# Kernel tuning notes

Hardware: AMD Instinct MI355X
Metric: run time of the kernel (lower is better)

## Reference

```python
import jax, jax.numpy as jnp
import numpy as np

GRID = 128      # voxel grid extent per axis
NUM_BATCH = 4
N_PER = 25000   # points per scene (unique voxels)
C = 128
K = 32          # number of classes in probs
HEADS = 8
SCALE = 1.0


def setup_inputs() -> dict:
    key = jax.random.key(0)
    ks = jax.random.split(key, 12)
    N = NUM_BATCH * N_PER
    # unique voxel coordinates per scene (submanifold conv assumes no duplicate sites)
    coords_list = []
    for b in range(NUM_BATCH):
        flat = jax.random.permutation(jax.random.fold_in(ks[0], b), GRID ** 3)[:N_PER]
        xyz = jnp.stack([flat // (GRID * GRID), (flat // GRID) % GRID, flat % GRID], axis=1)
        bcol = jnp.full((N_PER, 1), b)
        coords_list.append(jnp.concatenate([bcol, xyz], axis=1))
    coords = jnp.concatenate(coords_list, axis=0).astype(jnp.int32)  # [N,4] = (b,x,y,z)
    feats = jax.random.normal(ks[1], (N, C), jnp.float32)
    probs = jax.random.normal(ks[2], (N, K), jnp.float32)
    conv_w = jax.random.normal(ks[3], (27, C, C), jnp.float32) * (1.0 / np.sqrt(27 * C))
    bn_gamma = 1.0 + 0.1 * jax.random.normal(ks[4], (C,), jnp.float32)
    bn_beta = 0.1 * jax.random.normal(ks[5], (C,), jnp.float32)
    in_proj_w = jax.random.normal(ks[6], (3 * C, C), jnp.float32) / np.sqrt(C)
    in_proj_b = 0.01 * jax.random.normal(ks[7], (3 * C,), jnp.float32)
    out_proj_w = jax.random.normal(ks[8], (C, C), jnp.float32) / np.sqrt(C)
    out_proj_b = 0.01 * jax.random.normal(ks[9], (C,), jnp.float32)
    bottleneck_w = jax.random.normal(ks[10], (C, 2 * C), jnp.float32) / np.sqrt(2 * C)
    return {"feats": feats, "probs": probs, "conv_w": conv_w, "bn_gamma": bn_gamma,
            "bn_beta": bn_beta, "in_proj_w": in_proj_w, "in_proj_b": in_proj_b,
            "out_proj_w": out_proj_w, "out_proj_b": out_proj_b,
            "bottleneck_w": bottleneck_w, "coords": coords, "batch_size": NUM_BATCH}


def _subm_conv3x3(feats, coords, conv_w, batch_size):
    """Submanifold 3x3x3 sparse conv: outputs only at active sites, gathering active neighbors."""
    N = feats.shape[0]
    b, xyz = coords[:, 0], coords[:, 1:]
    grid = jnp.full((batch_size, GRID, GRID, GRID), -1, jnp.int32)
    grid = grid.at[b, xyz[:, 0], xyz[:, 1], xyz[:, 2]].set(jnp.arange(N, dtype=jnp.int32))
    out = jnp.zeros((N, conv_w.shape[-1]), feats.dtype)
    kidx = 0
    for dx in (-1, 0, 1):
        for dy in (-1, 0, 1):
            for dz in (-1, 0, 1):
                nb = xyz + jnp.array([dx, dy, dz], jnp.int32)
                inb = jnp.all((nb >= 0) & (nb < GRID), axis=1)
                nbc = jnp.clip(nb, 0, GRID - 1)
                j = grid[b, nbc[:, 0], nbc[:, 1], nbc[:, 2]]
                ok = inb & (j >= 0)
                g = jnp.where(ok[:, None], feats[jnp.maximum(j, 0)], 0.0)
                out = out + g @ conv_w[kidx]
                kidx += 1
    return out


def _forward(feats, probs, conv_w, bn_gamma, bn_beta, in_proj_w, in_proj_b,
             out_proj_w, out_proj_b, bottleneck_w, coords, batch_size):
    N, Cc = feats.shape
    dh = Cc // HEADS
    b = coords[:, 0]
    # transform_input: SubMConv3d -> BatchNorm1d (batch stats) -> ReLU
    x = _subm_conv3x3(feats, coords, conv_w, batch_size)
    mu = jnp.mean(x, axis=0)
    var = jnp.var(x, axis=0)
    x = jax.nn.relu((x - mu) * jax.lax.rsqrt(var + 1e-5) * bn_gamma + bn_beta)
    # SpatialGatherModule: per-scene softmax over points, soft-weighted context [B,K,C]
    m = b[None, :] == jnp.arange(batch_size, dtype=b.dtype)[:, None]          # [B,N]
    neg = jnp.finfo(x.dtype).min
    z = jnp.where(m[:, :, None], (SCALE * probs)[None], neg)                  # [B,N,K]
    w = jax.nn.softmax(z, axis=1)
    ctx = jnp.einsum('bnk,nc->bkc', w, x)                                     # [B,K,C]
    # per-scene MultiheadAttention (unbatched): query = points, key/value = context
    Wq, Wk, Wv = in_proj_w[:Cc], in_proj_w[Cc:2 * Cc], in_proj_w[2 * Cc:]
    bq, bk, bv = in_proj_b[:Cc], in_proj_b[Cc:2 * Cc], in_proj_b[2 * Cc:]
    q = ((x @ Wq.T + bq) * (dh ** -0.5)).reshape(N, HEADS, dh)
    kh = (ctx @ Wk.T + bk).reshape(batch_size, -1, HEADS, dh)
    vh = (ctx @ Wv.T + bv).reshape(batch_size, -1, HEADS, dh)
    scores = jnp.einsum('nhd,bkhd->nbhk', q, kh)
    scores = scores[jnp.arange(N), b]                                         # [N,H,K] pick own scene
    attn = jax.nn.softmax(scores, axis=-1)
    o = jnp.einsum('nhk,bkhd->nbhd', attn, vh)[jnp.arange(N), b]              # [N,H,dh]
    attn_out = o.reshape(N, Cc) @ out_proj_w.T + out_proj_b
    # torch code aliases feats with inputs.features, so the in-place scatter makes
    # both halves of the concat equal to attn_out (literal forward semantics)
    y = jnp.concatenate([attn_out, attn_out], axis=1) @ bottleneck_w.T
    return y


def reference(feats, probs, conv_w, bn_gamma, bn_beta, in_proj_w, in_proj_b,
              out_proj_w, out_proj_b, bottleneck_w, coords, batch_size):
    return _forward(feats, probs, conv_w, bn_gamma, bn_beta, in_proj_w, in_proj_b,
                    out_proj_w, out_proj_b, bottleneck_w, coords, batch_size)
```

## Files before the change

kernel.cpp:

```cpp
#include <hip/hip_runtime.h>
#include <hip/hip_bf16.h>

typedef __attribute__((ext_vector_type(8))) short short8;
typedef __attribute__((ext_vector_type(4))) float floatx4;

#define NB 4
#define GRIDD 128
#define GRID3 (128*128*128)
#define C 128
#define KSLOT 32
#define CTX_BPB 256
#define DEN_BLK 1024
#define STAT_BLK 1024
#define PCAP 8192

static __device__ __forceinline__ unsigned short f2bf(float f){
  unsigned u = __builtin_bit_cast(unsigned, f);
  unsigned r = (u + 0x7FFFu + ((u >> 16) & 1u)) >> 16;
  return (unsigned short)r;
}
static __device__ __forceinline__ float bf2f(unsigned short h){
  unsigned u = ((unsigned)h) << 16;
  return __builtin_bit_cast(float, u);
}

__global__ void prepk(const float* __restrict__ feats, const float* __restrict__ convw,
                      const float* __restrict__ inw,
                      unsigned short* __restrict__ Fb, unsigned short* __restrict__ Wt,
                      unsigned short* __restrict__ Wq, unsigned short* __restrict__ WkvT,
                      long total1)
{
  const long stride = (long)gridDim.x * blockDim.x;
  const long i0 = (long)blockIdx.x * blockDim.x + threadIdx.x;
  const long q4 = total1 >> 2;
  const float4* f4 = reinterpret_cast<const float4*>(feats);
  ushort4* fb4 = reinterpret_cast<ushort4*>(Fb);
  for (long i = i0; i < q4; i += stride){
    const float4 v = f4[i];
    ushort4 o; o.x = f2bf(v.x); o.y = f2bf(v.y); o.z = f2bf(v.z); o.w = f2bf(v.w);
    fb4[i] = o;
  }
  for (long i = i0; i < 27L*C*C; i += stride){
    long k = i >> 14; long r = (i >> 7) & 127; long c = i & 127;
    Wt[i] = f2bf(convw[(k << 14) + (c << 7) + r]);
  }
  for (long i = i0; i < C*C; i += stride) Wq[i] = f2bf(inw[i]);
  for (long i = i0; i < 2L*C*C; i += stride){
    long which = i >> 14, rem = i & 16383, ii = rem >> 7, cout = rem & 127;
    WkvT[i] = f2bf(inw[((1 + which) << 14) + (cout << 7) + ii]);
  }
}

__global__ __launch_bounds__(128) void w2k(const float* __restrict__ bw,
                                           const float* __restrict__ outw,
                                           const float* __restrict__ outb,
                                           unsigned short* __restrict__ W2b,
                                           float* __restrict__ b2){
  const int o = blockIdx.x, i = threadIdx.x;
  __shared__ float wcf[128];
  __shared__ float red[128];
  const float w_i = bw[(size_t)o*256 + i] + bw[(size_t)o*256 + 128 + i];
  wcf[i] = w_i;
  red[i] = w_i * outb[i];
  __syncthreads();
  float acc = 0.f;
  #pragma unroll 8
  for (int j = 0; j < 128; j++) acc = fmaf(wcf[j], outw[j*128 + i], acc);
  W2b[o*128 + i] = f2bf(acc);
  for (int s = 64; s > 0; s >>= 1){
    if (i < s) red[i] += red[i + s];
    __syncthreads();
  }
  if (i == 0) b2[o] = red[0];
}

__global__ void scatterk(const int* __restrict__ coords, int* __restrict__ gh, int N){
  int p = blockIdx.x * 256 + threadIdx.x;
  if (p < N){
    int4 cr = *reinterpret_cast<const int4*>(coords + (size_t)p * 4);
    gh[(((cr.x*GRIDD + cr.y)*GRIDD + cr.z)*GRIDD) + cr.w] = p;
  }
}

__global__ __launch_bounds__(256) void pairk(const int* __restrict__ coords,
                                             const int* __restrict__ gh,
                                             int2* __restrict__ pairs,
                                             int* __restrict__ gcnt, int N){
  __shared__ int wcnt[4][27];
  __shared__ int woff[4][27];
  const int t = threadIdx.x, wave = t >> 6, lane = t & 63;
  const int p = blockIdx.x * 256 + t;
  const bool active = p < N;
  int4 cr = make_int4(0, 0, 0, 0);
  if (active) cr = *reinterpret_cast<const int4*>(coords + (size_t)p * 4);
  const int b = cr.x, x = cr.y, y = cr.z, z = cr.w;
  int jl[27];
  #pragma unroll
  for (int k = 0; k < 27; k++){
    jl[k] = -1;
    if (k == 13) continue;
    if (active){
      const int dx = k / 9 - 1, dy = (k / 3) % 3 - 1, dz = k % 3 - 1;
      const int nx = x + dx, ny = y + dy, nz = z + dz;
      if (((unsigned)nx < 128u) & ((unsigned)ny < 128u) & ((unsigned)nz < 128u)){
        const int gi = ((((b << 7) + nx) << 7) + ny) * GRIDD + nz;
        const int jj = gh[gi];
        if ((unsigned)jj < (unsigned)N){
          const int4 cj = *reinterpret_cast<const int4*>(coords + (size_t)jj * 4);
          if (cj.x == b && cj.y == nx && cj.z == ny && cj.w == nz) jl[k] = jj;
        }
      }
    }
  }
  #pragma unroll
  for (int k = 0; k < 27; k++){
    const unsigned long long m = __ballot(jl[k] >= 0);
    if (lane == 0) wcnt[wave][k] = (int)__popcll(m);
  }
  __syncthreads();
  if (t < 27){
    const int c0 = wcnt[0][t], c1 = wcnt[1][t], c2 = wcnt[2][t], c3 = wcnt[3][t];
    const int tot = c0 + c1 + c2 + c3;
    int gb = 0;
    if (t != 13 && tot > 0) gb = atomicAdd(&gcnt[t], tot);
    woff[0][t] = gb;
    woff[1][t] = gb + c0;
    woff[2][t] = gb + c0 + c1;
    woff[3][t] = gb + c0 + c1 + c2;
  }
  __syncthreads();
  const unsigned long long ltm = ((unsigned long long)1 << lane) - 1;
  #pragma unroll
  for (int k = 0; k < 27; k++){
    if (k == 13) continue;
    const unsigned long long m = __ballot(jl[k] >= 0);
    if (jl[k] >= 0){
      const int slot = woff[wave][k] + (int)__popcll(m & ltm);
      if (slot < PCAP) pairs[(size_t)k * PCAP + slot] = make_int2(p, jl[k]);
    }
  }
}

__global__ __launch_bounds__(256) void scatk(
    const unsigned short* __restrict__ F, const unsigned short* __restrict__ Wt,
    const int2* __restrict__ pairs, const int* __restrict__ gcnt,
    float* __restrict__ X, int N)
{
  __shared__ unsigned short wl[128 * 136];
  const int k = (blockIdx.x < 13) ? blockIdx.x : blockIdx.x + 1;
  const int t = threadIdx.x;
  const unsigned short* wg = Wt + (size_t)k * C * C;
  for (int idx = t; idx < 128 * 16; idx += 256){
    const int row = idx >> 4, seg = idx & 15;
    *reinterpret_cast<short8*>(&wl[row * 136 + seg * 8]) =
        *reinterpret_cast<const short8*>(wg + row * 128 + seg * 8);
  }
  __syncthreads();
  const int cnt = min(gcnt[k], PCAP);
  const int nch = (cnt + 15) >> 4;
  const int wave = t >> 6, lane = t & 63, lo = lane & 15, hi = lane >> 4;
  for (int c = blockIdx.y * 4 + wave; c < nch; c += 32 * 4){
    const int pidx = c * 16 + lo;
    const bool pv = pidx < cnt;
    const int2 pr = pv ? pairs[(size_t)k * PCAP + pidx] : make_int2(0, 0);
    const unsigned short* frow = F + (size_t)pr.y * C;
    short8 a[4];
    #pragma unroll
    for (int kc = 0; kc < 4; kc++){
      a[kc] = *reinterpret_cast<const short8*>(frow + kc * 32 + hi * 8);
      if (!pv) a[kc] = (short8){0,0,0,0,0,0,0,0};
    }
    floatx4 acc[8];
    #pragma unroll
    for (int i = 0; i < 8; i++) acc[i] = (floatx4){0.f,0.f,0.f,0.f};
    #pragma unroll
    for (int kc = 0; kc < 4; kc++){
      const int koff = kc * 32 + hi * 8;
      #pragma unroll
      for (int ct = 0; ct < 8; ct++){
        const short8 b = *reinterpret_cast<const short8*>(&wl[(ct*16 + lo) * 136 + koff]);
        acc[ct] = __builtin_amdgcn_mfma_f32_16x16x32_bf16(a[kc], b, acc[ct], 0, 0, 0);
      }
    }
    #pragma unroll
    for (int i2 = 0; i2 < 4; i2++){
      const int src = hi * 4 + i2;
      const int row = __shfl(pr.x, src);
      if (c * 16 + src < cnt){
        #pragma unroll
        for (int ct = 0; ct < 8; ct++)
          atomicAdd(&X[(size_t)row * C + ct * 16 + lo], acc[ct][i2]);
      }
    }
  }
}

__global__ __launch_bounds__(256) void denomk(const float* __restrict__ probs,
                                              const int* __restrict__ coords,
                                              float* __restrict__ dpart, int N){
  const int t = threadIdx.x, k = t & 31, rh = t >> 5;
  float a0 = 0.f, a1 = 0.f, a2 = 0.f, a3 = 0.f;
  for (int r = blockIdx.x * 8 + rh; r < N; r += DEN_BLK * 8){
    const int b = coords[(size_t)r * 4];
    const float e = __expf(probs[(size_t)r * 32 + k]);
    a0 += (b == 0) ? e : 0.f;
    a1 += (b == 1) ? e : 0.f;
    a2 += (b == 2) ? e : 0.f;
    a3 += (b == 3) ? e : 0.f;
  }
  __shared__ float ls[8][128];
  ls[rh][0*32 + k] = a0; ls[rh][1*32 + k] = a1;
  ls[rh][2*32 + k] = a2; ls[rh][3*32 + k] = a3;
  __syncthreads();
  if (t < 128){
    float s = 0.f;
    #pragma unroll
    for (int j = 0; j < 8; j++) s += ls[j][t];
    dpart[(size_t)blockIdx.x * 128 + t] = s;
  }
}

__global__ __launch_bounds__(256) void statsk(const float* __restrict__ X,
                                              float* __restrict__ spgs, int N){
  const int t = threadIdx.x, c4 = t & 31, rg = t >> 5;
  float s0=0.f,s1=0.f,s2=0.f,s3=0.f, q0=0.f,q1=0.f,q2=0.f,q3=0.f;
  for (int r = blockIdx.x * 8 + rg; r < N; r += STAT_BLK * 8){
    const float4 v = *reinterpret_cast<const float4*>(X + (size_t)r * C + c4 * 4);
    s0 += v.x; s1 += v.y; s2 += v.z; s3 += v.w;
    q0 = fmaf(v.x, v.x, q0); q1 = fmaf(v.y, v.y, q1);
    q2 = fmaf(v.z, v.z, q2); q3 = fmaf(v.w, v.w, q3);
  }
  __shared__ float ls[256][4], lq[256][4];
  ls[t][0]=s0; ls[t][1]=s1; ls[t][2]=s2; ls[t][3]=s3;
  lq[t][0]=q0; lq[t][1]=q1; lq[t][2]=q2; lq[t][3]=q3;
  __syncthreads();
  if (t < 32){
    float as[4]={0.f,0.f,0.f,0.f}, aq[4]={0.f,0.f,0.f,0.f};
    #pragma unroll
    for (int g = 0; g < 8; g++){
      #pragma unroll
      for (int j = 0; j < 4; j++){ as[j] += ls[g*32 + t][j]; aq[j] += lq[g*32 + t][j]; }
    }
    #pragma unroll
    for (int j = 0; j < 4; j++){
      spgs[(size_t)blockIdx.x * 256 + t*4 + j] = as[j];
      spgs[(size_t)blockIdx.x * 256 + 128 + t*4 + j] = aq[j];
    }
  }
}

__global__ __launch_bounds__(128) void reduk(const float* __restrict__ pgs,
                                             const float* __restrict__ dpart,
                                             float* __restrict__ gsum,
                                             float* __restrict__ gsq,
                                             float* __restrict__ denom){
  const int which = blockIdx.x, slice = blockIdx.y, t = threadIdx.x;
  float s = 0.f;
  if (which < 2){
    const float* src = pgs + which * 128 + t;
    for (int j = slice; j < STAT_BLK; j += 8) s += src[(size_t)j * 256];
    atomicAdd((which ? gsq : gsum) + t, s);
  } else {
    const float* src = dpart + t;
    for (int j = slice; j < DEN_BLK; j += 8) s += src[(size_t)j * 128];
    atomicAdd(denom + t, s);
  }
}

__global__ void finalizek(const float* __restrict__ sums, const float* __restrict__ sumsq,
                          const float* __restrict__ gamma, const float* __restrict__ beta,
                          const float* __restrict__ denom,
                          float* __restrict__ scalev, float* __restrict__ shiftv,
                          float* __restrict__ invden, int N){
  const int t = threadIdx.x;
  const float invN = 1.f / (float)N;
  const float mu = sums[t] * invN;
  const float var = sumsq[t] * invN - mu * mu;
  const float sc = gamma[t] * rsqrtf(var + 1e-5f);
  scalev[t] = sc;
  shiftv[t] = beta[t] - mu * sc;
  invden[t] = 1.f / denom[t];
}

__global__ __launch_bounds__(256) void ctx2k(const float* __restrict__ Xm,
                                             const float* __restrict__ probs,
                                             const float* __restrict__ scalev,
                                             const float* __restrict__ shiftv,
                                             float* __restrict__ pbuf, int NPER){
  __shared__ float xL[32 * 128];
  __shared__ float pe[32 * 32];
  __shared__ float red[2 * KSLOT * C];
  const int blk = blockIdx.x;
  const int b = blk >> 8, j = blk & 255;
  const int rows = (NPER + CTX_BPB - 1) / CTX_BPB;
  const int r0 = j * rows;
  const int r1 = min(r0 + rows, NPER);
  const int t = threadIdx.x, c = t & 127, rh = t >> 7;
  const float sc = scalev[c], sh = shiftv[c];
  float acc[KSLOT];
  #pragma unroll
  for (int k = 0; k < KSLOT; k++) acc[k] = 0.f;

  for (int base = r0; base < r1; base += 32){
    __syncthreads();
    #pragma unroll
    for (int i = 0; i < 4; i++){
      const int idx = i * 256 + t;
      const int r = idx >> 5, c4 = idx & 31;
      const int rr = base + r;
      float4 v = make_float4(0.f, 0.f, 0.f, 0.f);
      if (rr < r1) v = *reinterpret_cast<const float4*>(Xm + ((size_t)b * NPER + rr) * C + c4 * 4);
      *reinterpret_cast<float4*>(&xL[r * 128 + c4 * 4]) = v;
    }
    {
      const int r = t >> 3, k4 = t & 7;
      const int rr = base + r;
      float4 v = make_float4(0.f, 0.f, 0.f, 0.f);
      if (rr < r1){
        const float4 pv = *reinterpret_cast<const float4*>(probs + ((size_t)b * NPER + rr) * 32 + k4 * 4);
        v.x = __expf(pv.x); v.y = __expf(pv.y); v.z = __expf(pv.z); v.w = __expf(pv.w);
      }
      *reinterpret_cast<float4*>(&pe[r * 32 + k4 * 4]) = v;
    }
    __syncthreads();
    const int rend = min(32, r1 - base);
    for (int r = rh; r < rend; r += 2){
      const float xv = fmaxf(fmaf(xL[r * 128 + c], sc, sh), 0.f);
      const float4* wr = reinterpret_cast<const float4*>(&pe[r * 32]);
      #pragma unroll
      for (int kq = 0; kq < 8; kq++){
        const float4 w4 = wr[kq];
        acc[kq*4+0] = fmaf(w4.x, xv, acc[kq*4+0]);
        acc[kq*4+1] = fmaf(w4.y, xv, acc[kq*4+1]);
        acc[kq*4+2] = fmaf(w4.z, xv, acc[kq*4+2]);
        acc[kq*4+3] = fmaf(w4.w, xv, acc[kq*4+3]);
      }
    }
  }
  __syncthreads();
  #pragma unroll
  for (int k = 0; k < KSLOT; k++) red[(rh * KSLOT + k) * C + c] = acc[k];
  __syncthreads();
  float* dst = pbuf + (size_t)blk * KSLOT * C;
  for (int i = t; i < KSLOT * C; i += 256) dst[i] = red[i] + red[KSLOT * C + i];
}

__global__ __launch_bounds__(256) void kvk(const float* __restrict__ pbuf,
                                           const float* __restrict__ invden,
                                           const unsigned short* __restrict__ WkvT,
                                           const float* __restrict__ inb,
                                           float* __restrict__ kh, float* __restrict__ vh){
  __shared__ float rowp[2][C];
  __shared__ float row[C];
  const int bk = blockIdx.x;
  const int b = bk >> 5, k = bk & 31;
  const int t = threadIdx.x, c = t & 127, jh = t >> 7;
  float s = 0.f;
  for (int j = jh; j < CTX_BPB; j += 2)
    s += pbuf[((size_t)(b * CTX_BPB + j) * KSLOT + k) * C + c];
  rowp[jh][c] = s;
  __syncthreads();
  if (t < C) row[t] = (rowp[0][t] + rowp[1][t]) * invden[b * KSLOT + k];
  __syncthreads();
  const int which = t >> 7;
  const unsigned short* W = WkvT + (size_t)which * C * C;
  float acc = inb[(1 + which) * C + c];
  #pragma unroll 8
  for (int i = 0; i < C; i++) acc = fmaf(row[i], bf2f(W[i * C + c]), acc);
  (which ? vh : kh)[(size_t)bk * C + c] = acc;
}

__global__ __launch_bounds__(256) void gemm128(
    const unsigned short* __restrict__ A, const unsigned short* __restrict__ W,
    const float* __restrict__ bias, float scale,
    float* __restrict__ outF, unsigned short* __restrict__ outB, int N)
{
  const int tid = threadIdx.x;
  const int wave = tid >> 6, lane = tid & 63;
  const int rbase = blockIdx.x * 64 + (wave >> 1) * 32;
  const int cbase = (wave & 1) * 64;
  const int lo = lane & 15, hi = lane >> 4;
  floatx4 acc[2][4];
  #pragma unroll
  for (int rt = 0; rt < 2; rt++)
    #pragma unroll
    for (int ct = 0; ct < 4; ct++) acc[rt][ct] = (floatx4){0.f,0.f,0.f,0.f};
  const int m0 = rbase + lo, m1 = rbase + 16 + lo;
  const int m0c = m0 < N ? m0 : N - 1;
  const int m1c = m1 < N ? m1 : N - 1;
  #pragma unroll
  for (int kc = 0; kc < 4; kc++){
    const int koff = kc * 32 + hi * 8;
    const short8 a0 = *reinterpret_cast<const short8*>(A + (size_t)m0c * C + koff);
    const short8 a1 = *reinterpret_cast<const short8*>(A + (size_t)m1c * C + koff);
    #pragma unroll
    for (int ct = 0; ct < 4; ct++){
      const int n = cbase + ct * 16 + lo;
      const short8 b = *reinterpret_cast<const short8*>(W + (size_t)n * C + koff);
      acc[0][ct] = __builtin_amdgcn_mfma_f32_16x16x32_bf16(a0, b, acc[0][ct], 0, 0, 0);
      acc[1][ct] = __builtin_amdgcn_mfma_f32_16x16x32_bf16(a1, b, acc[1][ct], 0, 0, 0);
    }
  }
  #pragma unroll
  for (int rt = 0; rt < 2; rt++){
    #pragma unroll
    for (int ct = 0; ct < 4; ct++){
      const int col = cbase + ct * 16 + lo;
      const float bv = bias ? bias[col] : 0.f;
      #pragma unroll
      for (int i = 0; i < 4; i++){
        const int row = rbase + rt * 16 + hi * 4 + i;
        if (row < N){
          const float v = (acc[rt][ct][i] + bv) * scale;
          if (outF) outF[(size_t)row * C + col] = v;
          if (outB) outB[(size_t)row * C + col] = f2bf(v);
        }
      }
    }
  }
}

__global__ __launch_bounds__(256) void gemm128f(
    const float* __restrict__ A, const unsigned short* __restrict__ W,
    const float* __restrict__ bias, const float* __restrict__ bnsc,
    const float* __restrict__ bnsh, float scale,
    unsigned short* __restrict__ outB, int N)
{
  const int tid = threadIdx.x;
  const int wave = tid >> 6, lane = tid & 63;
  const int rbase = blockIdx.x * 64 + (wave >> 1) * 32;
  const int cbase = (wave & 1) * 64;
  const int lo = lane & 15, hi = lane >> 4;
  floatx4 acc[2][4];
  #pragma unroll
  for (int rt = 0; rt < 2; rt++)
    #pragma unroll
    for (int ct = 0; ct < 4; ct++) acc[rt][ct] = (floatx4){0.f,0.f,0.f,0.f};
  const int m0 = rbase + lo, m1 = rbase + 16 + lo;
  const int m0c = m0 < N ? m0 : N - 1;
  const int m1c = m1 < N ? m1 : N - 1;
  #pragma unroll
  for (int kc = 0; kc < 4; kc++){
    const int koff = kc * 32 + hi * 8;
    short8 a0, a1;
    #pragma unroll
    for (int half = 0; half < 2; half++){
      const float4 sc = *reinterpret_cast<const float4*>(bnsc + koff + half * 4);
      const float4 sh = *reinterpret_cast<const float4*>(bnsh + koff + half * 4);
      const float4 x0 = *reinterpret_cast<const float4*>(A + (size_t)m0c * C + koff + half * 4);
      const float4 x1 = *reinterpret_cast<const float4*>(A + (size_t)m1c * C + koff + half * 4);
      const float* scp = &sc.x; const float* shp = &sh.x;
      const float* x0p = &x0.x; const float* x1p = &x1.x;
      #pragma unroll
      for (int j = 0; j < 4; j++){
        a0[half*4 + j] = (short)f2bf(fmaxf(fmaf(x0p[j], scp[j], shp[j]), 0.f));
        a1[half*4 + j] = (short)f2bf(fmaxf(fmaf(x1p[j], scp[j], shp[j]), 0.f));
      }
    }
    #pragma unroll
    for (int ct = 0; ct < 4; ct++){
      const int n = cbase + ct * 16 + lo;
      const short8 b = *reinterpret_cast<const short8*>(W + (size_t)n * C + koff);
      acc[0][ct] = __builtin_amdgcn_mfma_f32_16x16x32_bf16(a0, b, acc[0][ct], 0, 0, 0);
      acc[1][ct] = __builtin_amdgcn_mfma_f32_16x16x32_bf16(a1, b, acc[1][ct], 0, 0, 0);
    }
  }
  #pragma unroll
  for (int rt = 0; rt < 2; rt++){
    #pragma unroll
    for (int ct = 0; ct < 4; ct++){
      const int col = cbase + ct * 16 + lo;
      const float bv = bias[col];
      #pragma unroll
      for (int i = 0; i < 4; i++){
        const int row = rbase + rt * 16 + hi * 4 + i;
        if (row < N) outB[(size_t)row * C + col] = f2bf((acc[rt][ct][i] + bv) * scale);
      }
    }
  }
}

__global__ __launch_bounds__(256) void attn3k(const unsigned short* __restrict__ qb,
                                              const float* __restrict__ kh,
                                              const float* __restrict__ vh,
                                              unsigned short* __restrict__ ob, int NPER){
  __shared__ float khL[KSLOT * C];
  __shared__ float vhL[KSLOT * C];
  const int t = threadIdx.x;
  const int b = blockIdx.y;
  const int n0 = blockIdx.x * 64;
  {
    const float4* ks = reinterpret_cast<const float4*>(kh + (size_t)b * KSLOT * C);
    const float4* vs = reinterpret_cast<const float4*>(vh + (size_t)b * KSLOT * C);
    float4* kd = reinterpret_cast<float4*>(khL);
    float4* vd = reinterpret_cast<float4*>(vhL);
    #pragma unroll
    for (int i = 0; i < 4; i++){ kd[i * 256 + t] = ks[i * 256 + t]; vd[i * 256 + t] = vs[i * 256 + t]; }
  }
  __syncthreads();
  const int h = t >> 5, p = t & 31;
  for (int g = 0; g < 2; g++){
    const int n = n0 + g * 32 + p;
    const int nc = n < NPER ? n : NPER - 1;
    float qv[16];
    {
      const short8* qp = reinterpret_cast<const short8*>(qb + ((size_t)b * NPER + nc) * C + h * 16);
      const short8 qa = qp[0], qc = qp[1];
      #pragma unroll
      for (int i = 0; i < 8; i++){
        qv[i]     = bf2f((unsigned short)qa[i]);
        qv[8 + i] = bf2f((unsigned short)qc[i]);
      }
    }
    float sv[KSLOT];
    #pragma unroll
    for (int k = 0; k < KSLOT; k++){
      const float4* kp = reinterpret_cast<const float4*>(&khL[k * C + h * 16]);
      const float4 k0 = kp[0], k1 = kp[1], k2 = kp[2], k3 = kp[3];
      float s;
      s = qv[0] * k0.x;
      s = fmaf(qv[1], k0.y, s);  s = fmaf(qv[2],  k0.z, s);  s = fmaf(qv[3],  k0.w, s);
      s = fmaf(qv[4], k1.x, s);  s = fmaf(qv[5],  k1.y, s);  s = fmaf(qv[6],  k1.z, s);
      s = fmaf(qv[7], k1.w, s);  s = fmaf(qv[8],  k2.x, s);  s = fmaf(qv[9],  k2.y, s);
      s = fmaf(qv[10], k2.z, s); s = fmaf(qv[11], k2.w, s);  s = fmaf(qv[12], k3.x, s);
      s = fmaf(qv[13], k3.y, s); s = fmaf(qv[14], k3.z, s);  s = fmaf(qv[15], k3.w, s);
      sv[k] = s;
    }
    float m = sv[0];
    #pragma unroll
    for (int k = 1; k < KSLOT; k++) m = fmaxf(m, sv[k]);
    float sum = 0.f;
    #pragma unroll
    for (int k = 0; k < KSLOT; k++){ const float e = __expf(sv[k] - m); sv[k] = e; sum += e; }
    const float inv = 1.f / sum;
    float o[16];
    #pragma unroll
    for (int i = 0; i < 16; i++) o[i] = 0.f;
    #pragma unroll
    for (int k = 0; k < KSLOT; k++){
      const float w = sv[k];
      const float4* vp = reinterpret_cast<const float4*>(&vhL[k * C + h * 16]);
      const float4 v0 = vp[0], v1 = vp[1], v2 = vp[2], v3 = vp[3];
      o[0]  = fmaf(w, v0.x, o[0]);  o[1]  = fmaf(w, v0.y, o[1]);
      o[2]  = fmaf(w, v0.z, o[2]);  o[3]  = fmaf(w, v0.w, o[3]);
      o[4]  = fmaf(w, v1.x, o[4]);  o[5]  = fmaf(w, v1.y, o[5]);
      o[6]  = fmaf(w, v1.z, o[6]);  o[7]  = fmaf(w, v1.w, o[7]);
      o[8]  = fmaf(w, v2.x, o[8]);  o[9]  = fmaf(w, v2.y, o[9]);
      o[10] = fmaf(w, v2.z, o[10]); o[11] = fmaf(w, v2.w, o[11]);
      o[12] = fmaf(w, v3.x, o[12]); o[13] = fmaf(w, v3.y, o[13]);
      o[14] = fmaf(w, v3.z, o[14]); o[15] = fmaf(w, v3.w, o[15]);
    }
    if (n < NPER){
      short8 s0, s1;
      #pragma unroll
      for (int i = 0; i < 8; i++){
        s0[i] = (short)f2bf(o[i] * inv);
        s1[i] = (short)f2bf(o[8 + i] * inv);
      }
      unsigned short* op = ob + ((size_t)b * NPER + n) * C + h * 16;
      *reinterpret_cast<short8*>(op) = s0;
      *reinterpret_cast<short8*>(op + 8) = s1;
    }
  }
}

extern "C" void kernel_launch(void* const* d_in, const int* in_sizes, int n_in,
                              void* d_out, int out_size, void* d_ws, size_t ws_size,
                              hipStream_t stream){
  const float* feats  = (const float*)d_in[0];
  const float* probs  = (const float*)d_in[1];
  const float* convw  = (const float*)d_in[2];
  const float* gamma  = (const float*)d_in[3];
  const float* beta   = (const float*)d_in[4];
  const float* inw    = (const float*)d_in[5];
  const float* inb    = (const float*)d_in[6];
  const float* outw   = (const float*)d_in[7];
  const float* outb   = (const float*)d_in[8];
  const float* bw     = (const float*)d_in[9];
  const int*   coords = (const int*)d_in[10];
  const int N = in_sizes[0] / C;
  const int NPER = N / NB;
  const int NBLK = (N + 63) / 64;

  char* ws = (char*)d_ws;
  size_t off = 0;
  auto alloc = [&](size_t bytes) -> char* {
    char* r = ws + off; off += (bytes + 255) & ~(size_t)255; return r;
  };
  int* grid_h            = (int*)alloc((size_t)NB * GRID3 * 4);
  unsigned short* featsb = (unsigned short*)alloc((size_t)N * C * 2);
  unsigned short* convwt = (unsigned short*)alloc((size_t)27 * C * C * 2);
  unsigned short* wq     = (unsigned short*)alloc((size_t)C * C * 2);
  unsigned short* wkvT   = (unsigned short*)alloc((size_t)2 * C * C * 2);
  unsigned short* w2b    = (unsigned short*)alloc((size_t)C * C * 2);
  float* b2              = (float*)alloc(512);
  float* xconv           = (float*)alloc((size_t)N * C * 4);
  unsigned short* qb     = (unsigned short*)alloc((size_t)N * C * 2);
  int2* pairs            = (int2*)alloc((size_t)27 * PCAP * 8);
  float* spgs            = (float*)alloc((size_t)STAT_BLK * 256 * 4);
  float* dpart           = (float*)alloc((size_t)DEN_BLK * 128 * 4);
  float* zero_base       = (float*)alloc((size_t)512 * 4);
  float* gsum   = zero_base;
  float* gsq    = zero_base + 128;
  float* denom  = zero_base + 256;
  int*   gcnt   = (int*)(zero_base + 384);
  float* invden = (float*)alloc(512);
  float* scalev = (float*)alloc(512);
  float* shiftv = (float*)alloc(512);
  float* kh     = (float*)alloc((size_t)NB * KSLOT * C * 4);
  float* vh     = (float*)alloc((size_t)NB * KSLOT * C * 4);
  float* pbuf = (float*)grid_h;
  unsigned short* o_bf = featsb;

  (void)hipMemsetAsync(zero_base, 0, (size_t)512 * 4, stream);
  prepk<<<2048, 256, 0, stream>>>(feats, convw, inw, featsb, convwt, wq, wkvT, (long)N * C);
  w2k<<<128, 128, 0, stream>>>(bw, outw, outb, w2b, b2);
  scatterk<<<(N + 255) / 256, 256, 0, stream>>>(coords, grid_h, N);
  pairk<<<(N + 255) / 256, 256, 0, stream>>>(coords, grid_h, pairs, gcnt, N);
  denomk<<<DEN_BLK, 256, 0, stream>>>(probs, coords, dpart, N);
  gemm128<<<NBLK, 256, 0, stream>>>(featsb, convwt + 13 * C * C, nullptr, 1.f, xconv, nullptr, N);
  scatk<<<dim3(26, 32), 256, 0, stream>>>(featsb, convwt, pairs, gcnt, xconv, N);
  statsk<<<STAT_BLK, 256, 0, stream>>>(xconv, spgs, N);
  {
    dim3 rg(3, 8);
    reduk<<<rg, 128, 0, stream>>>(spgs, dpart, gsum, gsq, denom);
  }
  finalizek<<<1, 128, 0, stream>>>(gsum, gsq, gamma, beta, denom, scalev, shiftv, invden, N);
  ctx2k<<<NB * CTX_BPB, 256, 0, stream>>>(xconv, probs, scalev, shiftv, pbuf, NPER);
  kvk<<<NB * KSLOT, 256, 0, stream>>>(pbuf, invden, wkvT, inb, kh, vh);
  gemm128f<<<NBLK, 256, 0, stream>>>(xconv, wq, inb, scalev, shiftv, 0.25f, qb, N);
  dim3 agrid((NPER + 63) / 64, NB);
  attn3k<<<agrid, 256, 0, stream>>>(qb, kh, vh, o_bf, NPER);
  gemm128<<<NBLK, 256, 0, stream>>>(o_bf, w2b, b2, 1.f, (float*)d_out, nullptr, N);
}
```

Measured before the change: 456.2 us.

## Emit bf16 copy of conv output in stats pass; interleave two queries in attention

The stats kernel now writes a bf16 copy of the conv output while it reads it. The context and Q-projection kernels then read this half-width copy instead of the fp32 tensor, which cuts the global traffic of those two later passes. The attention kernel also processes both query rows per thread at once, so each K/V value loaded from LDS is used twice and the dependent FMA chains run side by side. The cost is an extra write in statsk, bf16 rounding before batch-norm in ctx and Q, and higher register pressure in attention.

Result: slower. 1.183 ms (+159.3%).

```diff
diff --git a/kernel.cpp b/kernel.cpp
--- a/kernel.cpp
+++ b/kernel.cpp
@@ -221,11 +221,14 @@
 }
 
 __global__ __launch_bounds__(256) void statsk(const float* __restrict__ X,
-                                              float* __restrict__ spgs, int N){
+                                              float* __restrict__ spgs,
+                                              unsigned short* __restrict__ Xb, int N){
   const int t = threadIdx.x, c4 = t & 31, rg = t >> 5;
   float s0=0.f,s1=0.f,s2=0.f,s3=0.f, q0=0.f,q1=0.f,q2=0.f,q3=0.f;
   for (int r = blockIdx.x * 8 + rg; r < N; r += STAT_BLK * 8){
     const float4 v = *reinterpret_cast<const float4*>(X + (size_t)r * C + c4 * 4);
+    ushort4 o; o.x = f2bf(v.x); o.y = f2bf(v.y); o.z = f2bf(v.z); o.w = f2bf(v.w);
+    *reinterpret_cast<ushort4*>(Xb + (size_t)r * C + c4 * 4) = o;
     s0 += v.x; s1 += v.y; s2 += v.z; s3 += v.w;
     q0 = fmaf(v.x, v.x, q0); q1 = fmaf(v.y, v.y, q1);
     q2 = fmaf(v.z, v.z, q2); q3 = fmaf(v.w, v.w, q3);
@@ -282,7 +285,7 @@
   invden[t] = 1.f / denom[t];
 }
 
-__global__ __launch_bounds__(256) void ctx2k(const float* __restrict__ Xm,
+__global__ __launch_bounds__(256) void ctx2k(const unsigned short* __restrict__ Xb,
                                              const float* __restrict__ probs,
                                              const float* __restrict__ scalev,
                                              const float* __restrict__ shiftv,
@@ -304,13 +307,19 @@
   for (int base = r0; base < r1; base += 32){
     __syncthreads();
     #pragma unroll
-    for (int i = 0; i < 4; i++){
+    for (int i = 0; i < 2; i++){
       const int idx = i * 256 + t;
-      const int r = idx >> 5, c4 = idx & 31;
+      const int r = idx >> 4, c8 = idx & 15;
       const int rr = base + r;
-      float4 v = make_float4(0.f, 0.f, 0.f, 0.f);
-      if (rr < r1) v = *reinterpret_cast<const float4*>(Xm + ((size_t)b * NPER + rr) * C + c4 * 4);
-      *reinterpret_cast<float4*>(&xL[r * 128 + c4 * 4]) = v;
+      short8 v = (short8){0,0,0,0,0,0,0,0};
+      if (rr < r1) v = *reinterpret_cast<const short8*>(Xb + ((size_t)b * NPER + rr) * C + c8 * 8);
+      float4 f0, f1;
+      f0.x = bf2f((unsigned short)v[0]); f0.y = bf2f((unsigned short)v[1]);
+      f0.z = bf2f((unsigned short)v[2]); f0.w = bf2f((unsigned short)v[3]);
+      f1.x = bf2f((unsigned short)v[4]); f1.y = bf2f((unsigned short)v[5]);
+      f1.z = bf2f((unsigned short)v[6]); f1.w = bf2f((unsigned short)v[7]);
+      *reinterpret_cast<float4*>(&xL[r * 128 + c8 * 8]) = f0;
+      *reinterpret_cast<float4*>(&xL[r * 128 + c8 * 8 + 4]) = f1;
     }
     {
       const int r = t >> 3, k4 = t & 7;
@@ -420,8 +429,8 @@
   }
 }
 
-__global__ __launch_bounds__(256) void gemm128f(
-    const float* __restrict__ A, const unsigned short* __restrict__ W,
+__global__ __launch_bounds__(256) void gemm128b(
+    const unsigned short* __restrict__ A, const unsigned short* __restrict__ W,
     const float* __restrict__ bias, const float* __restrict__ bnsc,
     const float* __restrict__ bnsh, float scale,
     unsigned short* __restrict__ outB, int N)
@@ -442,20 +451,13 @@
   #pragma unroll
   for (int kc = 0; kc < 4; kc++){
     const int koff = kc * 32 + hi * 8;
-    short8 a0, a1;
-    #pragma unroll
-    for (int half = 0; half < 2; half++){
-      const float4 sc = *reinterpret_cast<const float4*>(bnsc + koff + half * 4);
-      const float4 sh = *reinterpret_cast<const float4*>(bnsh + koff + half * 4);
-      const float4 x0 = *reinterpret_cast<const float4*>(A + (size_t)m0c * C + koff + half * 4);
-      const float4 x1 = *reinterpret_cast<const float4*>(A + (size_t)m1c * C + koff + half * 4);
-      const float* scp = &sc.x; const float* shp = &sh.x;
-      const float* x0p = &x0.x; const float* x1p = &x1.x;
-      #pragma unroll
-      for (int j = 0; j < 4; j++){
-        a0[half*4 + j] = (short)f2bf(fmaxf(fmaf(x0p[j], scp[j], shp[j]), 0.f));
-        a1[half*4 + j] = (short)f2bf(fmaxf(fmaf(x1p[j], scp[j], shp[j]), 0.f));
-      }
+    short8 a0 = *reinterpret_cast<const short8*>(A + (size_t)m0c * C + koff);
+    short8 a1 = *reinterpret_cast<const short8*>(A + (size_t)m1c * C + koff);
+    #pragma unroll
+    for (int j = 0; j < 8; j++){
+      const float scj = bnsc[koff + j], shj = bnsh[koff + j];
+      a0[j] = (short)f2bf(fmaxf(fmaf(bf2f((unsigned short)a0[j]), scj, shj), 0.f));
+      a1[j] = (short)f2bf(fmaxf(fmaf(bf2f((unsigned short)a1[j]), scj, shj), 0.f));
     }
     #pragma unroll
     for (int ct = 0; ct < 4; ct++){
@@ -480,7 +482,7 @@
   }
 }
 
-__global__ __launch_bounds__(256) void attn3k(const unsigned short* __restrict__ qb,
+__global__ __launch_bounds__(256) void attn4k(const unsigned short* __restrict__ qb,
                                               const float* __restrict__ kh,
                                               const float* __restrict__ vh,
                                               unsigned short* __restrict__ ob, int NPER){
@@ -499,68 +501,103 @@
   }
   __syncthreads();
   const int h = t >> 5, p = t & 31;
-  for (int g = 0; g < 2; g++){
-    const int n = n0 + g * 32 + p;
-    const int nc = n < NPER ? n : NPER - 1;
-    float qv[16];
-    {
-      const short8* qp = reinterpret_cast<const short8*>(qb + ((size_t)b * NPER + nc) * C + h * 16);
-      const short8 qa = qp[0], qc = qp[1];
-      #pragma unroll
-      for (int i = 0; i < 8; i++){
-        qv[i]     = bf2f((unsigned short)qa[i]);
-        qv[8 + i] = bf2f((unsigned short)qc[i]);
-      }
-    }
-    float sv[KSLOT];
-    #pragma unroll
-    for (int k = 0; k < KSLOT; k++){
-      const float4* kp = reinterpret_cast<const float4*>(&khL[k * C + h * 16]);
-      const float4 k0 = kp[0], k1 = kp[1], k2 = kp[2], k3 = kp[3];
-      float s;
-      s = qv[0] * k0.x;
-      s = fmaf(qv[1], k0.y, s);  s = fmaf(qv[2],  k0.z, s);  s = fmaf(qv[3],  k0.w, s);
-      s = fmaf(qv[4], k1.x, s);  s = fmaf(qv[5],  k1.y, s);  s = fmaf(qv[6],  k1.z, s);
-      s = fmaf(qv[7], k1.w, s);  s = fmaf(qv[8],  k2.x, s);  s = fmaf(qv[9],  k2.y, s);
-      s = fmaf(qv[10], k2.z, s); s = fmaf(qv[11], k2.w, s);  s = fmaf(qv[12], k3.x, s);
-      s = fmaf(qv[13], k3.y, s); s = fmaf(qv[14], k3.z, s);  s = fmaf(qv[15], k3.w, s);
-      sv[k] = s;
-    }
-    float m = sv[0];
-    #pragma unroll
-    for (int k = 1; k < KSLOT; k++) m = fmaxf(m, sv[k]);
-    float sum = 0.f;
-    #pragma unroll
-    for (int k = 0; k < KSLOT; k++){ const float e = __expf(sv[k] - m); sv[k] = e; sum += e; }
-    const float inv = 1.f / sum;
-    float o[16];
-    #pragma unroll
-    for (int i = 0; i < 16; i++) o[i] = 0.f;
-    #pragma unroll
-    for (int k = 0; k < KSLOT; k++){
-      const float w = sv[k];
-      const float4* vp = reinterpret_cast<const float4*>(&vhL[k * C + h * 16]);
-      const float4 v0 = vp[0], v1 = vp[1], v2 = vp[2], v3 = vp[3];
-      o[0]  = fmaf(w, v0.x, o[0]);  o[1]  = fmaf(w, v0.y, o[1]);
-      o[2]  = fmaf(w, v0.z, o[2]);  o[3]  = fmaf(w, v0.w, o[3]);
-      o[4]  = fmaf(w, v1.x, o[4]);  o[5]  = fmaf(w, v1.y, o[5]);
-      o[6]  = fmaf(w, v1.z, o[6]);  o[7]  = fmaf(w, v1.w, o[7]);
-      o[8]  = fmaf(w, v2.x, o[8]);  o[9]  = fmaf(w, v2.y, o[9]);
-      o[10] = fmaf(w, v2.z, o[10]); o[11] = fmaf(w, v2.w, o[11]);
-      o[12] = fmaf(w, v3.x, o[12]); o[13] = fmaf(w, v3.y, o[13]);
-      o[14] = fmaf(w, v3.z, o[14]); o[15] = fmaf(w, v3.w, o[15]);
-    }
-    if (n < NPER){
-      short8 s0, s1;
-      #pragma unroll
-      for (int i = 0; i < 8; i++){
-        s0[i] = (short)f2bf(o[i] * inv);
-        s1[i] = (short)f2bf(o[8 + i] * inv);
-      }
-      unsigned short* op = ob + ((size_t)b * NPER + n) * C + h * 16;
-      *reinterpret_cast<short8*>(op) = s0;
-      *reinterpret_cast<short8*>(op + 8) = s1;
-    }
+  const int na = n0 + p, nb = n0 + 32 + p;
+  const int nac = na < NPER ? na : NPER - 1;
+  const int nbc = nb < NPER ? nb : NPER - 1;
+  float qa[16], qv[16];
+  {
+    const short8* qp = reinterpret_cast<const short8*>(qb + ((size_t)b * NPER + nac) * C + h * 16);
+    const short8 x0 = qp[0], x1 = qp[1];
+    const short8* qq = reinterpret_cast<const short8*>(qb + ((size_t)b * NPER + nbc) * C + h * 16);
+    const short8 y0 = qq[0], y1 = qq[1];
+    #pragma unroll
+    for (int i = 0; i < 8; i++){
+      qa[i] = bf2f((unsigned short)x0[i]); qa[8+i] = bf2f((unsigned short)x1[i]);
+      qv[i] = bf2f((unsigned short)y0[i]); qv[8+i] = bf2f((unsigned short)y1[i]);
+    }
+  }
+  float sa[KSLOT], sb[KSLOT];
+  #pragma unroll
+  for (int k = 0; k < KSLOT; k++){
+    const float4* kp = reinterpret_cast<const float4*>(&khL[k * C + h * 16]);
+    const float4 k0 = kp[0], k1 = kp[1], k2 = kp[2], k3 = kp[3];
+    const float* kf = &k0.x;
+    float s0 = 0.f, s1 = 0.f;
+    s0 = fmaf(qa[0], k0.x, s0); s1 = fmaf(qv[0], k0.x, s1);
+    s0 = fmaf(qa[1], k0.y, s0); s1 = fmaf(qv[1], k0.y, s1);
+    s0 = fmaf(qa[2], k0.z, s0); s1 = fmaf(qv[2], k0.z, s1);
+    s0 = fmaf(qa[3], k0.w, s0); s1 = fmaf(qv[3], k0.w, s1);
+    s0 = fmaf(qa[4], k1.x, s0); s1 = fmaf(qv[4], k1.x, s1);
+    s0 = fmaf(qa[5], k1.y, s0); s1 = fmaf(qv[5], k1.y, s1);
+    s0 = fmaf(qa[6], k1.z, s0); s1 = fmaf(qv[6], k1.z, s1);
+    s0 = fmaf(qa[7], k1.w, s0); s1 = fmaf(qv[7], k1.w, s1);
+    s0 = fmaf(qa[8], k2.x, s0); s1 = fmaf(qv[8], k2.x, s1);
+    s0 = fmaf(qa[9], k2.y, s0); s1 = fmaf(qv[9], k2.y, s1);
+    s0 = fmaf(qa[10], k2.z, s0); s1 = fmaf(qv[10], k2.z, s1);
+    s0 = fmaf(qa[11], k2.w, s0); s1 = fmaf(qv[11], k2.w, s1);
+    s0 = fmaf(qa[12], k3.x, s0); s1 = fmaf(qv[12], k3.x, s1);
+    s0 = fmaf(qa[13], k3.y, s0); s1 = fmaf(qv[13], k3.y, s1);
+    s0 = fmaf(qa[14], k3.z, s0); s1 = fmaf(qv[14], k3.z, s1);
+    s0 = fmaf(qa[15], k3.w, s0); s1 = fmaf(qv[15], k3.w, s1);
+    (void)kf;
+    sa[k] = s0; sb[k] = s1;
+  }
+  float ma = sa[0], mb = sb[0];
+  #pragma unroll
+  for (int k = 1; k < KSLOT; k++){ ma = fmaxf(ma, sa[k]); mb = fmaxf(mb, sb[k]); }
+  float suma = 0.f, sumb = 0.f;
+  #pragma unroll
+  for (int k = 0; k < KSLOT; k++){
+    const float ea = __expf(sa[k] - ma); sa[k] = ea; suma += ea;
+    const float eb = __expf(sb[k] - mb); sb[k] = eb; sumb += eb;
+  }
+  const float inva = 1.f / suma, invb = 1.f / sumb;
+  float oa[16], obv[16];
+  #pragma unroll
+  for (int i = 0; i < 16; i++){ oa[i] = 0.f; obv[i] = 0.f; }
+  #pragma unroll
+  for (int k = 0; k < KSLOT; k++){
+    const float wa = sa[k], wb = sb[k];
+    const float4* vp = reinterpret_cast<const float4*>(&vhL[k * C + h * 16]);
+    const float4 v0 = vp[0], v1 = vp[1], v2 = vp[2], v3 = vp[3];
+    oa[0]  = fmaf(wa, v0.x, oa[0]);  obv[0]  = fmaf(wb, v0.x, obv[0]);
+    oa[1]  = fmaf(wa, v0.y, oa[1]);  obv[1]  = fmaf(wb, v0.y, obv[1]);
+    oa[2]  = fmaf(wa, v0.z, oa[2]);  obv[2]  = fmaf(wb, v0.z, obv[2]);
+    oa[3]  = fmaf(wa, v0.w, oa[3]);  obv[3]  = fmaf(wb, v0.w, obv[3]);
+    oa[4]  = fmaf(wa, v1.x, oa[4]);  obv[4]  = fmaf(wb, v1.x, obv[4]);
+    oa[5]  = fmaf(wa, v1.y, oa[5]);  obv[5]  = fmaf(wb, v1.y, obv[5]);
+    oa[6]  = fmaf(wa, v1.z, oa[6]);  obv[6]  = fmaf(wb, v1.z, obv[6]);
+    oa[7]  = fmaf(wa, v1.w, oa[7]);  obv[7]  = fmaf(wb, v1.w, obv[7]);
+    oa[8]  = fmaf(wa, v2.x, oa[8]);  obv[8]  = fmaf(wb, v2.x, obv[8]);
+    oa[9]  = fmaf(wa, v2.y, oa[9]);  obv[9]  = fmaf(wb, v2.y, obv[9]);
+    oa[10] = fmaf(wa, v2.z, oa[10]); obv[10] = fmaf(wb, v2.z, obv[10]);
+    oa[11] = fmaf(wa, v2.w, oa[11]); obv[11] = fmaf(wb, v2.w, obv[11]);
+    oa[12] = fmaf(wa, v3.x, oa[12]); obv[12] = fmaf(wb, v3.x, obv[12]);
+    oa[13] = fmaf(wa, v3.y, oa[13]); obv[13] = fmaf(wb, v3.y, obv[13]);
+    oa[14] = fmaf(wa, v3.z, oa[14]); obv[14] = fmaf(wb, v3.z, obv[14]);
+    oa[15] = fmaf(wa, v3.w, oa[15]); obv[15] = fmaf(wb, v3.w, obv[15]);
+  }
+  if (na < NPER){
+    short8 s0, s1;
+    #pragma unroll
+    for (int i = 0; i < 8; i++){
+      s0[i] = (short)f2bf(oa[i] * inva);
+      s1[i] = (short)f2bf(oa[8 + i] * inva);
+    }
+    unsigned short* op = ob + ((size_t)b * NPER + na) * C + h * 16;
+    *reinterpret_cast<short8*>(op) = s0;
+    *reinterpret_cast<short8*>(op + 8) = s1;
+  }
+  if (nb < NPER){
+    short8 s0, s1;
+    #pragma unroll
+    for (int i = 0; i < 8; i++){
+      s0[i] = (short)f2bf(obv[i] * invb);
+      s1[i] = (short)f2bf(obv[8 + i] * invb);
+    }
+    unsigned short* op = ob + ((size_t)b * NPER + nb) * C + h * 16;
+    *reinterpret_cast<short8*>(op) = s0;
+    *reinterpret_cast<short8*>(op + 8) = s1;
   }
 }
 
@@ -610,6 +647,7 @@
   float* kh     = (float*)alloc((size_t)NB * KSLOT * C * 4);
   float* vh     = (float*)alloc((size_t)NB * KSLOT * C * 4);
   float* pbuf = (float*)grid_h;
+  unsigned short* xbf  = featsb;
   unsigned short* o_bf = featsb;
 
   (void)hipMemsetAsync(zero_base, 0, (size_t)512 * 4, stream);
@@ -620,16 +658,16 @@
   denomk<<<DEN_BLK, 256, 0, stream>>>(probs, coords, dpart, N);
   gemm128<<<NBLK, 256, 0, stream>>>(featsb, convwt + 13 * C * C, nullptr, 1.f, xconv, nullptr, N);
   scatk<<<dim3(26, 32), 256, 0, stream>>>(featsb, convwt, pairs, gcnt, xconv, N);
-  statsk<<<STAT_BLK, 256, 0, stream>>>(xconv, spgs, N);
+  statsk<<<STAT_BLK, 256, 0, stream>>>(xconv, spgs, xbf, N);
   {
     dim3 rg(3, 8);
     reduk<<<rg, 128, 0, stream>>>(spgs, dpart, gsum, gsq, denom);
   }
   finalizek<<<1, 128, 0, stream>>>(gsum, gsq, gamma, beta, denom, scalev, shiftv, invden, N);
-  ctx2k<<<NB * CTX_BPB, 256, 0, stream>>>(xconv, probs, scalev, shiftv, pbuf, NPER);
+  ctx2k<<<NB * CTX_BPB, 256, 0, stream>>>(xbf, probs, scalev, shiftv, pbuf, NPER);
   kvk<<<NB * KSLOT, 256, 0, stream>>>(pbuf, invden, wkvT, inb, kh, vh);
-  gemm128f<<<NBLK, 256, 0, stream>>>(xconv, wq, inb, scalev, shiftv, 0.25f, qb, N);
+  gemm128b<<<NBLK, 256, 0, stream>>>(xbf, wq, inb, scalev, shiftv, 0.25f, qb, N);
   dim3 agrid((NPER + 63) / 64, NB);
-  attn3k<<<agrid, 256, 0, stream>>>(qb, kh, vh, o_bf, NPER);
+  attn4k<<<agrid, 256, 0, stream>>>(qb, kh, vh, o_bf, NPER);
   gemm128<<<NBLK, 256, 0, stream>>>(o_bf, w2b, b2, 1.f, (float*)d_out, nullptr, N);
 }
```
